# Performance work log

Hardware: AMD Instinct MI355X
Metric: run time of the kernel (lower is better)

The kernel has to match this reference:

```python
import jax, jax.numpy as jnp
import numpy as np

N_NODES = 10000
N_EDGES = 640000
IN_DIM = 128
HID = 128
N_GRAPHS = 64


def setup_inputs() -> dict:
    key = jax.random.key(0)
    ks = jax.random.split(key, 9)
    x = jax.random.normal(ks[0], (N_NODES, IN_DIM), dtype=jnp.float32)
    edge_index = jax.random.randint(ks[1], (2, N_EDGES), 0, N_NODES, dtype=jnp.int32)
    batch = jnp.sort(jax.random.randint(ks[2], (N_NODES,), 0, N_GRAPHS, dtype=jnp.int32))
    # GCNConv weights (glorot-ish init) and zero biases
    W0 = jax.random.normal(ks[3], (IN_DIM, HID), dtype=jnp.float32) / np.float32(np.sqrt(IN_DIM))
    b0 = jnp.zeros((HID,), dtype=jnp.float32)
    W1 = jax.random.normal(ks[4], (HID, HID), dtype=jnp.float32) / np.float32(np.sqrt(HID))
    b1 = jnp.zeros((HID,), dtype=jnp.float32)
    W2 = jax.random.normal(ks[5], (HID, HID), dtype=jnp.float32) / np.float32(np.sqrt(HID))
    b2 = jnp.zeros((HID,), dtype=jnp.float32)
    return {"x": x, "edge_index": edge_index, "batch": batch,
            "W0": W0, "b0": b0, "W1": W1, "b1": b1, "W2": W2, "b2": b2}


def _gcn_conv(x, src, dst, W, b, n_nodes):
    """PyG GCNConv: self-loops + symmetric normalization, then linear+bias."""
    h = x @ W  # [N, H]
    # degree of destination nodes, +1 for the added self-loop
    deg = jax.ops.segment_sum(jnp.ones((src.shape[0],), h.dtype), dst,
                              num_segments=n_nodes) + 1.0
    dis = jax.lax.rsqrt(deg)  # deg >= 1 so no inf guard needed
    # messages along real edges, normalized by dis[src]*dis[dst]
    msg = h[src] * (dis[src] * dis[dst])[:, None]  # [E, H]
    out = jax.ops.segment_sum(msg, dst, num_segments=n_nodes)
    # self-loop contribution: dis[i]^2 * h[i]
    out = out + h * (dis * dis)[:, None]
    return out + b


def reference(x, edge_index, batch, W0, b0, W1, b1, W2, b2):
    src, dst = edge_index[0], edge_index[1]
    n_nodes = x.shape[0]
    # layer 0 and 1 followed by ReLU (dropout: eval mode -> identity)
    h = _gcn_conv(x, src, dst, W0, b0, n_nodes)
    h = jax.nn.relu(h)
    h = _gcn_conv(h, src, dst, W1, b1, n_nodes)
    h = jax.nn.relu(h)
    h = _gcn_conv(h, src, dst, W2, b2, n_nodes)
    # global mean pool over batch indices
    sums = jax.ops.segment_sum(h, batch, num_segments=N_GRAPHS)  # [B, H]
    counts = jax.ops.segment_sum(jnp.ones((n_nodes,), h.dtype), batch,
                                 num_segments=N_GRAPHS)
    return sums / jnp.maximum(counts, 1.0)[:, None]
```

## Files before the change

kernel.cpp:

```cpp
#include <hip/hip_runtime.h>
#include <hip/hip_fp16.h>

#define NN 10000
#define NE 640000
#define NG 64
#define CAP 128
#define NB 625
#define BCAP 1280

typedef _Float16 f16x8 __attribute__((ext_vector_type(8)));
typedef float f32x4 __attribute__((ext_vector_type(4)));

__global__ __launch_bounds__(256) void k_init(const int* __restrict__ batch,
                                              int* __restrict__ gstart,
                                              int* __restrict__ bcur,
                                              const float* __restrict__ W0,
                                              const float* __restrict__ W1,
                                              const float* __restrict__ W2,
                                              __half* __restrict__ wh,
                                              __half* __restrict__ wl) {
    int bid = blockIdx.x, t = threadIdx.x;
    if (bid < 40) {
        int i = bid * 256 + t;
        if (i < NB) bcur[i] = 0;
        if (i >= NN) return;
        int b = batch[i];
        int prev = (i == 0) ? -1 : batch[i - 1];
        for (int g = prev + 1; g <= b; g++) gstart[g] = i;
        if (i == NN - 1)
            for (int g = b + 1; g <= NG; g++) gstart[g] = NN;
        return;
    }
    int wid = bid - 40;
    int z = wid >> 6;
    int q = (wid & 63) * 256 + t;
    int c = q >> 7, k = q & 127;
    const float* W = (z == 0) ? W0 : (z == 1) ? W1 : W2;
    float v = W[k * 128 + c];
    __half h = __float2half(v);
    __half lo = __float2half(v - __half2float(h));
    wh[z * 16384 + c * 128 + k] = h;
    wl[z * 16384 + c * 128 + k] = lo;
}

__global__ __launch_bounds__(256) void k_p1(const int* __restrict__ ei,
                                            int* __restrict__ bcur,
                                            int* __restrict__ pk) {
    __shared__ int hist[NB];
    int t = threadIdx.x;
    for (int q = t; q < NB; q += 256) hist[q] = 0;
    __syncthreads();

    int4 s4[4], d4[4];
    int ebase = blockIdx.x * 4096;
#pragma unroll
    for (int q = 0; q < 4; q++) {
        int e = ebase + q * 1024 + t * 4;
        if (e < NE) {
            s4[q] = *(const int4*)&ei[e];
            d4[q] = *(const int4*)&ei[NE + e];
            atomicAdd(&hist[d4[q].x >> 4], 1);
            atomicAdd(&hist[d4[q].y >> 4], 1);
            atomicAdd(&hist[d4[q].z >> 4], 1);
            atomicAdd(&hist[d4[q].w >> 4], 1);
        }
    }
    __syncthreads();

    for (int q = t; q < NB; q += 256) {
        int h = hist[q];
        hist[q] = (h > 0) ? atomicAdd(&bcur[q], h) : 0;
    }
    __syncthreads();

#pragma unroll
    for (int q = 0; q < 4; q++) {
        int e = ebase + q * 1024 + t * 4;
        if (e < NE) {
            int b0 = d4[q].x >> 4, b1 = d4[q].y >> 4, b2 = d4[q].z >> 4, b3 = d4[q].w >> 4;
            int r0 = atomicAdd(&hist[b0], 1);
            int r1 = atomicAdd(&hist[b1], 1);
            int r2 = atomicAdd(&hist[b2], 1);
            int r3 = atomicAdd(&hist[b3], 1);
            if (r0 < BCAP) pk[b0 * BCAP + r0] = s4[q].x | ((d4[q].x & 15) << 14);
            if (r1 < BCAP) pk[b1 * BCAP + r1] = s4[q].y | ((d4[q].y & 15) << 14);
            if (r2 < BCAP) pk[b2 * BCAP + r2] = s4[q].z | ((d4[q].z & 15) << 14);
            if (r3 < BCAP) pk[b3 * BCAP + r3] = s4[q].w | ((d4[q].w & 15) << 14);
        }
    }
}

__global__ __launch_bounds__(256) void k_p2(const int* __restrict__ bcur,
                                            const int* __restrict__ pk,
                                            int* __restrict__ deg,
                                            int* __restrict__ csrc) {
    __shared__ int buf[16 * CAP];
    __shared__ int cnt[16];
    int b = blockIdx.x, t = threadIdx.x;
    if (t < 16) cnt[t] = 0;
    __syncthreads();

    int n = bcur[b];
    if (n > BCAP) n = BCAP;
    const int* pb = &pk[b * BCAP];
    for (int i = t; i < n; i += 256) {
        int v = pb[i];
        int nd = v >> 14;
        int slot = atomicAdd(&cnt[nd], 1);
        if (slot < CAP) buf[(nd << 7) + slot] = v & 0x3FFF;
    }
    __syncthreads();

    int node0 = b << 4;
    if (t < 16) {
        int c = cnt[t];
        deg[node0 + t] = c;
        buf[(t << 7) + min(c, CAP - 1)] = NN;
    }
    __syncthreads();

    int4* d4 = (int4*)&csrc[node0 << 7];
    const int4* s4 = (const int4*)buf;
#pragma unroll
    for (int i = 0; i < 2; i++) d4[t + i * 256] = s4[t + i * 256];
}

__global__ __launch_bounds__(256) void k_gemm(const float* __restrict__ in,
                                              const __half* __restrict__ whT,
                                              const __half* __restrict__ wlT,
                                              const int* __restrict__ deg,
                                              __half* __restrict__ g16, int relu) {
    int t = threadIdx.x;
    int w = t >> 6, l = t & 63;
    int rw = blockIdx.x * 32 + (w & 1) * 16;
    int cw = blockIdx.y * 64 + (w >> 1) * 32;
    int lr = l & 15, lg = l >> 4;
    int row = rw + lr;
    int rclamp = min(row, NN - 1);
    const _Float16* wh = (const _Float16*)whT;
    const _Float16* wl = (const _Float16*)wlT;
    f32x4 acc0 = {0.f, 0.f, 0.f, 0.f}, acc1 = {0.f, 0.f, 0.f, 0.f};
#pragma unroll
    for (int ks = 0; ks < 4; ks++) {
        int kb = ks * 32 + lg * 8;
        float4 xa = *(const float4*)&in[rclamp * 128 + kb];
        float4 xb = *(const float4*)&in[rclamp * 128 + kb + 4];
        float x0 = xa.x, x1 = xa.y, x2 = xa.z, x3 = xa.w;
        float x4 = xb.x, x5 = xb.y, x6 = xb.z, x7 = xb.w;
        if (relu) {
            x0 = fmaxf(x0, 0.f); x1 = fmaxf(x1, 0.f); x2 = fmaxf(x2, 0.f); x3 = fmaxf(x3, 0.f);
            x4 = fmaxf(x4, 0.f); x5 = fmaxf(x5, 0.f); x6 = fmaxf(x6, 0.f); x7 = fmaxf(x7, 0.f);
        }
        f16x8 ah, al;
        ah[0] = (_Float16)x0; al[0] = (_Float16)(x0 - (float)ah[0]);
        ah[1] = (_Float16)x1; al[1] = (_Float16)(x1 - (float)ah[1]);
        ah[2] = (_Float16)x2; al[2] = (_Float16)(x2 - (float)ah[2]);
        ah[3] = (_Float16)x3; al[3] = (_Float16)(x3 - (float)ah[3]);
        ah[4] = (_Float16)x4; al[4] = (_Float16)(x4 - (float)ah[4]);
        ah[5] = (_Float16)x5; al[5] = (_Float16)(x5 - (float)ah[5]);
        ah[6] = (_Float16)x6; al[6] = (_Float16)(x6 - (float)ah[6]);
        ah[7] = (_Float16)x7; al[7] = (_Float16)(x7 - (float)ah[7]);
        int c0 = cw + lr;
        f16x8 bh0 = *(const f16x8*)&wh[c0 * 128 + kb];
        f16x8 bl0 = *(const f16x8*)&wl[c0 * 128 + kb];
        f16x8 bh1 = *(const f16x8*)&wh[(c0 + 16) * 128 + kb];
        f16x8 bl1 = *(const f16x8*)&wl[(c0 + 16) * 128 + kb];
        acc0 = __builtin_amdgcn_mfma_f32_16x16x32_f16(ah, bh0, acc0, 0, 0, 0);
        acc1 = __builtin_amdgcn_mfma_f32_16x16x32_f16(ah, bh1, acc1, 0, 0, 0);
        acc0 = __builtin_amdgcn_mfma_f32_16x16x32_f16(al, bh0, acc0, 0, 0, 0);
        acc1 = __builtin_amdgcn_mfma_f32_16x16x32_f16(al, bh1, acc1, 0, 0, 0);
        acc0 = __builtin_amdgcn_mfma_f32_16x16x32_f16(ah, bl0, acc0, 0, 0, 0);
        acc1 = __builtin_amdgcn_mfma_f32_16x16x32_f16(ah, bl1, acc1, 0, 0, 0);
    }
#pragma unroll
    for (int reg = 0; reg < 4; reg++) {
        int r = rw + lg * 4 + reg;
        int c = cw + lr;
        if (r < NN) {
            float d = rsqrtf((float)deg[r] + 1.0f);
            g16[r * 128 + c] = __float2half(acc0[reg] * d);
            g16[r * 128 + c + 16] = __float2half(acc1[reg] * d);
        } else {
            g16[r * 128 + c] = __float2half(0.f);
            g16[r * 128 + c + 16] = __float2half(0.f);
        }
    }
}

__device__ __forceinline__ void accp(uint2 v, float2& p, float2& q) {
    float2 f0 = __half22float2(*(__half2*)&v.x);
    float2 f1 = __half22float2(*(__half2*)&v.y);
    p.x += f0.x; p.y += f0.y; q.x += f1.x; q.y += f1.y;
}

__global__ __launch_bounds__(256) void k_agg(const __half* __restrict__ g16,
                                             const float* __restrict__ bias,
                                             const int* __restrict__ deg,
                                             const int* __restrict__ csrc,
                                             float* __restrict__ out) {
    int wid = blockIdx.x * 4 + (threadIdx.x >> 6);
    int l = threadIdx.x & 63;
    if (wid >= NN) return;
    int i = wid;
    int dgi = __builtin_amdgcn_readfirstlane(deg[i]);
    int n = min(dgi, CAP - 1);
    int np = (n + 1) & ~1;
    int half = l >> 5, li = l & 31;
    int co = li * 4;
    float2 A0 = {0.f, 0.f}, A1 = {0.f, 0.f};
    float2 B0 = {0.f, 0.f}, B1 = {0.f, 0.f};
    if (half == 0) {
        uint2 sv = *(const uint2*)&g16[i * 128 + co];
        float2 f0 = __half22float2(*(__half2*)&sv.x);
        float2 f1 = __half22float2(*(__half2*)&sv.y);
        A0 = f0; A1 = f1;
    }
    const int* cp = &csrc[i << 7];
    for (int base = 0; base < np; base += 64) {
        int m = np - base;
        if (m > 64) m = 64;
        int myedge = (l < m) ? cp[base + l] : NN;
        int pairs = m >> 1;
        int j = 0;
        for (; j + 8 <= pairs; j += 8) {
            int r0 = __shfl(myedge, 2 * j + half);
            int r1 = __shfl(myedge, 2 * j + 2 + half);
            int r2 = __shfl(myedge, 2 * j + 4 + half);
            int r3 = __shfl(myedge, 2 * j + 6 + half);
            int r4 = __shfl(myedge, 2 * j + 8 + half);
            int r5 = __shfl(myedge, 2 * j + 10 + half);
            int r6 = __shfl(myedge, 2 * j + 12 + half);
            int r7 = __shfl(myedge, 2 * j + 14 + half);
            uint2 v0 = *(const uint2*)&g16[r0 * 128 + co];
            uint2 v1 = *(const uint2*)&g16[r1 * 128 + co];
            uint2 v2 = *(const uint2*)&g16[r2 * 128 + co];
            uint2 v3 = *(const uint2*)&g16[r3 * 128 + co];
            uint2 v4 = *(const uint2*)&g16[r4 * 128 + co];
            uint2 v5 = *(const uint2*)&g16[r5 * 128 + co];
            uint2 v6 = *(const uint2*)&g16[r6 * 128 + co];
            uint2 v7 = *(const uint2*)&g16[r7 * 128 + co];
            accp(v0, A0, A1); accp(v1, B0, B1);
            accp(v2, A0, A1); accp(v3, B0, B1);
            accp(v4, A0, A1); accp(v5, B0, B1);
            accp(v6, A0, A1); accp(v7, B0, B1);
        }
        for (; j < pairs; j++) {
            int r = __shfl(myedge, 2 * j + half);
            uint2 v = *(const uint2*)&g16[r * 128 + co];
            accp(v, A0, A1);
        }
    }
    A0.x += B0.x; A0.y += B0.y; A1.x += B1.x; A1.y += B1.y;
    A0.x += __shfl_xor(A0.x, 32);
    A0.y += __shfl_xor(A0.y, 32);
    A1.x += __shfl_xor(A1.x, 32);
    A1.y += __shfl_xor(A1.y, 32);
    if (half == 0) {
        float di = rsqrtf((float)dgi + 1.0f);
        float4 bb = *(const float4*)&bias[co];
        float4 o;
        o.x = di * A0.x + bb.x;
        o.y = di * A0.y + bb.y;
        o.z = di * A1.x + bb.z;
        o.w = di * A1.y + bb.w;
        *(float4*)&out[i * 128 + co] = o;
    }
}

__global__ __launch_bounds__(256) void k_pool(const float* __restrict__ h,
                                              const int* __restrict__ gstart,
                                              float* __restrict__ out) {
    int g = blockIdx.x;
    int s = gstart[g], e = gstart[g + 1];
    int t = threadIdx.x;
    int c = t & 127, half = t >> 7;
    float acc = 0.f;
    for (int n = s + half; n < e; n += 2) acc += h[n * 128 + c];
    __shared__ float sm[256];
    sm[t] = acc;
    __syncthreads();
    if (half == 0) {
        float cnt = (float)max(e - s, 1);
        out[g * 128 + c] = (sm[c] + sm[128 + c]) / cnt;
    }
}

extern "C" void kernel_launch(void* const* d_in, const int* in_sizes, int n_in,
                              void* d_out, int out_size, void* d_ws, size_t ws_size,
                              hipStream_t stream) {
    const float* x     = (const float*)d_in[0];
    const int*   ei    = (const int*)d_in[1];
    const int*   batch = (const int*)d_in[2];
    const float* W0 = (const float*)d_in[3];
    const float* b0 = (const float*)d_in[4];
    const float* W1 = (const float*)d_in[5];
    const float* b1 = (const float*)d_in[6];
    const float* W2 = (const float*)d_in[7];
    const float* b2 = (const float*)d_in[8];
    float* out = (float*)d_out;

    float* ws    = (float*)d_ws;
    int*   deg   = (int*)ws;
    int*   gstart= (int*)(ws + 10240);
    int*   bcur  = (int*)(ws + 10320);
    int*   csrc  = (int*)(ws + 10960);
    __half* g16  = (__half*)(ws + 1290960);
    float* abuf  = ws + 1931984;
    int*   pk    = (int*)(ws + 1931984);
    __half* wh   = (__half*)(ws + 3211984);
    __half* wlo  = (__half*)(ws + 3236560);

    k_init<<<232, 256, 0, stream>>>(batch, gstart, bcur, W0, W1, W2, wh, wlo);
    k_p1<<<157, 256, 0, stream>>>(ei, bcur, pk);
    k_p2<<<NB, 256, 0, stream>>>(bcur, pk, deg, csrc);

    dim3 ggrid(313, 2);
    k_gemm<<<ggrid, 256, 0, stream>>>(x, wh, wlo, deg, g16, 0);
    k_agg<<<2500, 256, 0, stream>>>(g16, b0, deg, csrc, abuf);
    k_gemm<<<ggrid, 256, 0, stream>>>(abuf, wh + 16384, wlo + 16384, deg, g16, 1);
    k_agg<<<2500, 256, 0, stream>>>(g16, b1, deg, csrc, abuf);
    k_gemm<<<ggrid, 256, 0, stream>>>(abuf, wh + 32768, wlo + 32768, deg, g16, 1);
    k_agg<<<2500, 256, 0, stream>>>(g16, b2, deg, csrc, abuf);

    k_pool<<<NG, 256, 0, stream>>>(abuf, gstart, out);
}
```

Before: 197.4 us.

## Fuse edge bucketing with init, CSR build with first GEMM, aggregation with next GEMM

The setup kernel now also does the edge-bucketing pass, and the per-bucket CSR build also runs the first layer's split-fp16 MFMA GEMM. A new fused kernel aggregates 16 nodes into shared memory, applies bias and ReLU, then multiplies by the next layer's weights. This cuts the launch count and removes the fp32 activation round trip through global memory between aggregation and GEMM. The price is larger 512-thread blocks, per-block dependence on the slowest node's aggregation before the GEMM, and ping-pong fp16 buffers with explicitly zeroed sentinel rows.

```diff
diff --git a/kernel.cpp b/kernel.cpp
--- a/kernel.cpp
+++ b/kernel.cpp
@@ -11,89 +11,95 @@
 typedef _Float16 f16x8 __attribute__((ext_vector_type(8)));
 typedef float f32x4 __attribute__((ext_vector_type(4)));
 
-__global__ __launch_bounds__(256) void k_init(const int* __restrict__ batch,
-                                              int* __restrict__ gstart,
-                                              int* __restrict__ bcur,
-                                              const float* __restrict__ W0,
-                                              const float* __restrict__ W1,
-                                              const float* __restrict__ W2,
-                                              __half* __restrict__ wh,
-                                              __half* __restrict__ wl) {
+__device__ __forceinline__ void split8v(float4 xa, float4 xb, f16x8& ah, f16x8& al) {
+    float x[8] = {xa.x, xa.y, xa.z, xa.w, xb.x, xb.y, xb.z, xb.w};
+#pragma unroll
+    for (int j = 0; j < 8; j++) {
+        ah[j] = (_Float16)x[j];
+        al[j] = (_Float16)(x[j] - (float)ah[j]);
+    }
+}
+
+__global__ __launch_bounds__(256) void k_initp1(
+    const int* __restrict__ batch, int* __restrict__ gstart,
+    const float* __restrict__ W0, const float* __restrict__ W1, const float* __restrict__ W2,
+    __half* __restrict__ wh, __half* __restrict__ wl,
+    const int* __restrict__ ei, int* __restrict__ bcur, int* __restrict__ pk,
+    __half* __restrict__ g16a, __half* __restrict__ g16b)
+{
+    __shared__ int hist[NB];
     int bid = blockIdx.x, t = threadIdx.x;
     if (bid < 40) {
         int i = bid * 256 + t;
-        if (i < NB) bcur[i] = 0;
-        if (i >= NN) return;
-        int b = batch[i];
-        int prev = (i == 0) ? -1 : batch[i - 1];
-        for (int g = prev + 1; g <= b; g++) gstart[g] = i;
-        if (i == NN - 1)
-            for (int g = b + 1; g <= NG; g++) gstart[g] = NN;
-        return;
-    }
-    int wid = bid - 40;
-    int z = wid >> 6;
-    int q = (wid & 63) * 256 + t;
-    int c = q >> 7, k = q & 127;
-    const float* W = (z == 0) ? W0 : (z == 1) ? W1 : W2;
-    float v = W[k * 128 + c];
-    __half h = __float2half(v);
-    __half lo = __float2half(v - __half2float(h));
-    wh[z * 16384 + c * 128 + k] = h;
-    wl[z * 16384 + c * 128 + k] = lo;
-}
-
-__global__ __launch_bounds__(256) void k_p1(const int* __restrict__ ei,
-                                            int* __restrict__ bcur,
-                                            int* __restrict__ pk) {
-    __shared__ int hist[NB];
-    int t = threadIdx.x;
-    for (int q = t; q < NB; q += 256) hist[q] = 0;
-    __syncthreads();
-
-    int4 s4[4], d4[4];
-    int ebase = blockIdx.x * 4096;
-#pragma unroll
-    for (int q = 0; q < 4; q++) {
-        int e = ebase + q * 1024 + t * 4;
-        if (e < NE) {
-            s4[q] = *(const int4*)&ei[e];
-            d4[q] = *(const int4*)&ei[NE + e];
-            atomicAdd(&hist[d4[q].x >> 4], 1);
-            atomicAdd(&hist[d4[q].y >> 4], 1);
-            atomicAdd(&hist[d4[q].z >> 4], 1);
-            atomicAdd(&hist[d4[q].w >> 4], 1);
-        }
-    }
-    __syncthreads();
-
-    for (int q = t; q < NB; q += 256) {
-        int h = hist[q];
-        hist[q] = (h > 0) ? atomicAdd(&bcur[q], h) : 0;
-    }
-    __syncthreads();
-
-#pragma unroll
-    for (int q = 0; q < 4; q++) {
-        int e = ebase + q * 1024 + t * 4;
-        if (e < NE) {
-            int b0 = d4[q].x >> 4, b1 = d4[q].y >> 4, b2 = d4[q].z >> 4, b3 = d4[q].w >> 4;
-            int r0 = atomicAdd(&hist[b0], 1);
-            int r1 = atomicAdd(&hist[b1], 1);
-            int r2 = atomicAdd(&hist[b2], 1);
-            int r3 = atomicAdd(&hist[b3], 1);
-            if (r0 < BCAP) pk[b0 * BCAP + r0] = s4[q].x | ((d4[q].x & 15) << 14);
-            if (r1 < BCAP) pk[b1 * BCAP + r1] = s4[q].y | ((d4[q].y & 15) << 14);
-            if (r2 < BCAP) pk[b2 * BCAP + r2] = s4[q].z | ((d4[q].z & 15) << 14);
-            if (r3 < BCAP) pk[b3 * BCAP + r3] = s4[q].w | ((d4[q].w & 15) << 14);
-        }
-    }
-}
-
-__global__ __launch_bounds__(256) void k_p2(const int* __restrict__ bcur,
-                                            const int* __restrict__ pk,
-                                            int* __restrict__ deg,
-                                            int* __restrict__ csrc) {
+        if (i < NN) {
+            int b = batch[i];
+            int prev = (i == 0) ? -1 : batch[i - 1];
+            for (int g = prev + 1; g <= b; g++) gstart[g] = i;
+            if (i == NN - 1)
+                for (int g = b + 1; g <= NG; g++) gstart[g] = NN;
+        }
+    } else if (bid < 232) {
+        int wid = bid - 40;
+        int z = wid >> 6;
+        int q = (wid & 63) * 256 + t;
+        int c = q >> 7, k = q & 127;
+        const float* W = (z == 0) ? W0 : (z == 1) ? W1 : W2;
+        float v = W[k * 128 + c];
+        __half h = __float2half(v);
+        __half lo = __float2half(v - __half2float(h));
+        wh[z * 16384 + c * 128 + k] = h;
+        wl[z * 16384 + c * 128 + k] = lo;
+    } else if (bid < 389) {
+        for (int q = t; q < NB; q += 256) hist[q] = 0;
+        __syncthreads();
+        int4 s4[4], d4[4];
+        int ebase = (bid - 232) * 4096;
+#pragma unroll
+        for (int q = 0; q < 4; q++) {
+            int e = ebase + q * 1024 + t * 4;
+            if (e < NE) {
+                s4[q] = *(const int4*)&ei[e];
+                d4[q] = *(const int4*)&ei[NE + e];
+                atomicAdd(&hist[d4[q].x >> 4], 1);
+                atomicAdd(&hist[d4[q].y >> 4], 1);
+                atomicAdd(&hist[d4[q].z >> 4], 1);
+                atomicAdd(&hist[d4[q].w >> 4], 1);
+            }
+        }
+        __syncthreads();
+        for (int q = t; q < NB; q += 256) {
+            int h = hist[q];
+            hist[q] = (h > 0) ? atomicAdd(&bcur[q], h) : 0;
+        }
+        __syncthreads();
+#pragma unroll
+        for (int q = 0; q < 4; q++) {
+            int e = ebase + q * 1024 + t * 4;
+            if (e < NE) {
+                int b0i = d4[q].x >> 4, b1i = d4[q].y >> 4, b2i = d4[q].z >> 4, b3i = d4[q].w >> 4;
+                int r0 = atomicAdd(&hist[b0i], 1);
+                int r1 = atomicAdd(&hist[b1i], 1);
+                int r2 = atomicAdd(&hist[b2i], 1);
+                int r3 = atomicAdd(&hist[b3i], 1);
+                if (r0 < BCAP) pk[b0i * BCAP + r0] = s4[q].x | ((d4[q].x & 15) << 14);
+                if (r1 < BCAP) pk[b1i * BCAP + r1] = s4[q].y | ((d4[q].y & 15) << 14);
+                if (r2 < BCAP) pk[b2i * BCAP + r2] = s4[q].z | ((d4[q].z & 15) << 14);
+                if (r3 < BCAP) pk[b3i * BCAP + r3] = s4[q].w | ((d4[q].w & 15) << 14);
+            }
+        }
+    } else {
+        uint4 z = {0u, 0u, 0u, 0u};
+        ((uint4*)(g16a + NN * 128))[t] = z;
+        ((uint4*)(g16b + NN * 128))[t] = z;
+    }
+}
+
+__global__ __launch_bounds__(512) void k_p2g0(
+    const int* __restrict__ bcur, const int* __restrict__ pk,
+    const float* __restrict__ x,
+    const __half* __restrict__ whT, const __half* __restrict__ wlT,
+    int* __restrict__ deg, int* __restrict__ csrc, __half* __restrict__ g16a)
+{
     __shared__ int buf[16 * CAP];
     __shared__ int cnt[16];
     int b = blockIdx.x, t = threadIdx.x;
@@ -103,7 +109,7 @@
     int n = bcur[b];
     if (n > BCAP) n = BCAP;
     const int* pb = &pk[b * BCAP];
-    for (int i = t; i < n; i += 256) {
+    for (int i = t; i < n; i += 512) {
         int v = pb[i];
         int nd = v >> 14;
         int slot = atomicAdd(&cnt[nd], 1);
@@ -119,71 +125,31 @@
     }
     __syncthreads();
 
-    int4* d4 = (int4*)&csrc[node0 << 7];
-    const int4* s4 = (const int4*)buf;
-#pragma unroll
-    for (int i = 0; i < 2; i++) d4[t + i * 256] = s4[t + i * 256];
-}
-
-__global__ __launch_bounds__(256) void k_gemm(const float* __restrict__ in,
-                                              const __half* __restrict__ whT,
-                                              const __half* __restrict__ wlT,
-                                              const int* __restrict__ deg,
-                                              __half* __restrict__ g16, int relu) {
-    int t = threadIdx.x;
-    int w = t >> 6, l = t & 63;
-    int rw = blockIdx.x * 32 + (w & 1) * 16;
-    int cw = blockIdx.y * 64 + (w >> 1) * 32;
-    int lr = l & 15, lg = l >> 4;
-    int row = rw + lr;
-    int rclamp = min(row, NN - 1);
-    const _Float16* wh = (const _Float16*)whT;
-    const _Float16* wl = (const _Float16*)wlT;
-    f32x4 acc0 = {0.f, 0.f, 0.f, 0.f}, acc1 = {0.f, 0.f, 0.f, 0.f};
+    ((int4*)&csrc[node0 << 7])[t] = ((const int4*)buf)[t];
+
+    int w = t >> 6, l = t & 63, lr = l & 15, lg = l >> 4;
+    int cw = w * 16;
+    const _Float16* whp = (const _Float16*)whT;
+    const _Float16* wlp = (const _Float16*)wlT;
+    f32x4 acc = {0.f, 0.f, 0.f, 0.f};
 #pragma unroll
     for (int ks = 0; ks < 4; ks++) {
         int kb = ks * 32 + lg * 8;
-        float4 xa = *(const float4*)&in[rclamp * 128 + kb];
-        float4 xb = *(const float4*)&in[rclamp * 128 + kb + 4];
-        float x0 = xa.x, x1 = xa.y, x2 = xa.z, x3 = xa.w;
-        float x4 = xb.x, x5 = xb.y, x6 = xb.z, x7 = xb.w;
-        if (relu) {
-            x0 = fmaxf(x0, 0.f); x1 = fmaxf(x1, 0.f); x2 = fmaxf(x2, 0.f); x3 = fmaxf(x3, 0.f);
-            x4 = fmaxf(x4, 0.f); x5 = fmaxf(x5, 0.f); x6 = fmaxf(x6, 0.f); x7 = fmaxf(x7, 0.f);
-        }
         f16x8 ah, al;
-        ah[0] = (_Float16)x0; al[0] = (_Float16)(x0 - (float)ah[0]);
-        ah[1] = (_Float16)x1; al[1] = (_Float16)(x1 - (float)ah[1]);
-        ah[2] = (_Float16)x2; al[2] = (_Float16)(x2 - (float)ah[2]);
-        ah[3] = (_Float16)x3; al[3] = (_Float16)(x3 - (float)ah[3]);
-        ah[4] = (_Float16)x4; al[4] = (_Float16)(x4 - (float)ah[4]);
-        ah[5] = (_Float16)x5; al[5] = (_Float16)(x5 - (float)ah[5]);
-        ah[6] = (_Float16)x6; al[6] = (_Float16)(x6 - (float)ah[6]);
-        ah[7] = (_Float16)x7; al[7] = (_Float16)(x7 - (float)ah[7]);
+        split8v(*(const float4*)&x[(node0 + lr) * 128 + kb],
+                *(const float4*)&x[(node0 + lr) * 128 + kb + 4], ah, al);
         int c0 = cw + lr;
-        f16x8 bh0 = *(const f16x8*)&wh[c0 * 128 + kb];
-        f16x8 bl0 = *(const f16x8*)&wl[c0 * 128 + kb];
-        f16x8 bh1 = *(const f16x8*)&wh[(c0 + 16) * 128 + kb];
-        f16x8 bl1 = *(const f16x8*)&wl[(c0 + 16) * 128 + kb];
-        acc0 = __builtin_amdgcn_mfma_f32_16x16x32_f16(ah, bh0, acc0, 0, 0, 0);
-        acc1 = __builtin_amdgcn_mfma_f32_16x16x32_f16(ah, bh1, acc1, 0, 0, 0);
-        acc0 = __builtin_amdgcn_mfma_f32_16x16x32_f16(al, bh0, acc0, 0, 0, 0);
-        acc1 = __builtin_amdgcn_mfma_f32_16x16x32_f16(al, bh1, acc1, 0, 0, 0);
-        acc0 = __builtin_amdgcn_mfma_f32_16x16x32_f16(ah, bl0, acc0, 0, 0, 0);
-        acc1 = __builtin_amdgcn_mfma_f32_16x16x32_f16(ah, bl1, acc1, 0, 0, 0);
+        f16x8 bh = *(const f16x8*)&whp[c0 * 128 + kb];
+        f16x8 bl = *(const f16x8*)&wlp[c0 * 128 + kb];
+        acc = __builtin_amdgcn_mfma_f32_16x16x32_f16(ah, bh, acc, 0, 0, 0);
+        acc = __builtin_amdgcn_mfma_f32_16x16x32_f16(al, bh, acc, 0, 0, 0);
+        acc = __builtin_amdgcn_mfma_f32_16x16x32_f16(ah, bl, acc, 0, 0, 0);
     }
 #pragma unroll
     for (int reg = 0; reg < 4; reg++) {
-        int r = rw + lg * 4 + reg;
-        int c = cw + lr;
-        if (r < NN) {
-            float d = rsqrtf((float)deg[r] + 1.0f);
-            g16[r * 128 + c] = __float2half(acc0[reg] * d);
-            g16[r * 128 + c + 16] = __float2half(acc1[reg] * d);
-        } else {
-            g16[r * 128 + c] = __float2half(0.f);
-            g16[r * 128 + c + 16] = __float2half(0.f);
-        }
+        int row = lg * 4 + reg;
+        float d = rsqrtf((float)cnt[row] + 1.0f);
+        g16a[(node0 + row) * 128 + cw + lr] = __float2half(acc[reg] * d);
     }
 }
 
@@ -191,6 +157,110 @@
     float2 f0 = __half22float2(*(__half2*)&v.x);
     float2 f1 = __half22float2(*(__half2*)&v.y);
     p.x += f0.x; p.y += f0.y; q.x += f1.x; q.y += f1.y;
+}
+
+__global__ __launch_bounds__(512) void k_ag(
+    const __half* __restrict__ gin, const float* __restrict__ bias,
+    const int* __restrict__ deg, const int* __restrict__ csrc,
+    const __half* __restrict__ whT, const __half* __restrict__ wlT,
+    __half* __restrict__ gout)
+{
+    __shared__ float Xs[16][132];
+    int base = blockIdx.x << 4;
+    int t = threadIdx.x;
+    int w = t >> 6, l = t & 63;
+    int half = l >> 5, li = l & 31;
+    int co = li * 4;
+#pragma unroll
+    for (int k4 = 0; k4 < 2; k4++) {
+        int row = w * 2 + k4;
+        int i = base + row;
+        int dgi = __builtin_amdgcn_readfirstlane(deg[i]);
+        int nn_ = min(dgi, CAP - 1);
+        int np = (nn_ + 1) & ~1;
+        float2 A0 = {0.f, 0.f}, A1 = {0.f, 0.f};
+        float2 B0 = {0.f, 0.f}, B1 = {0.f, 0.f};
+        if (half == 0) {
+            uint2 sv = *(const uint2*)&gin[i * 128 + co];
+            A0 = __half22float2(*(__half2*)&sv.x);
+            A1 = __half22float2(*(__half2*)&sv.y);
+        }
+        const int* cp = &csrc[i << 7];
+        for (int bs = 0; bs < np; bs += 64) {
+            int m = np - bs;
+            if (m > 64) m = 64;
+            int myedge = (l < m) ? cp[bs + l] : NN;
+            int pairs = m >> 1;
+            int j = 0;
+            for (; j + 8 <= pairs; j += 8) {
+                int r0 = __shfl(myedge, 2 * j + half);
+                int r1 = __shfl(myedge, 2 * j + 2 + half);
+                int r2 = __shfl(myedge, 2 * j + 4 + half);
+                int r3 = __shfl(myedge, 2 * j + 6 + half);
+                int r4 = __shfl(myedge, 2 * j + 8 + half);
+                int r5 = __shfl(myedge, 2 * j + 10 + half);
+                int r6 = __shfl(myedge, 2 * j + 12 + half);
+                int r7 = __shfl(myedge, 2 * j + 14 + half);
+                uint2 v0 = *(const uint2*)&gin[r0 * 128 + co];
+                uint2 v1 = *(const uint2*)&gin[r1 * 128 + co];
+                uint2 v2 = *(const uint2*)&gin[r2 * 128 + co];
+                uint2 v3 = *(const uint2*)&gin[r3 * 128 + co];
+                uint2 v4 = *(const uint2*)&gin[r4 * 128 + co];
+                uint2 v5 = *(const uint2*)&gin[r5 * 128 + co];
+                uint2 v6 = *(const uint2*)&gin[r6 * 128 + co];
+                uint2 v7 = *(const uint2*)&gin[r7 * 128 + co];
+                accp(v0, A0, A1); accp(v1, B0, B1);
+                accp(v2, A0, A1); accp(v3, B0, B1);
+                accp(v4, A0, A1); accp(v5, B0, B1);
+                accp(v6, A0, A1); accp(v7, B0, B1);
+            }
+            for (; j < pairs; j++) {
+                int r = __shfl(myedge, 2 * j + half);
+                uint2 v = *(const uint2*)&gin[r * 128 + co];
+                accp(v, A0, A1);
+            }
+        }
+        A0.x += B0.x; A0.y += B0.y; A1.x += B1.x; A1.y += B1.y;
+        A0.x += __shfl_xor(A0.x, 32);
+        A0.y += __shfl_xor(A0.y, 32);
+        A1.x += __shfl_xor(A1.x, 32);
+        A1.y += __shfl_xor(A1.y, 32);
+        if (half == 0) {
+            float di = rsqrtf((float)dgi + 1.0f);
+            float4 bb = *(const float4*)&bias[co];
+            float4 o;
+            o.x = fmaxf(di * A0.x + bb.x, 0.f);
+            o.y = fmaxf(di * A0.y + bb.y, 0.f);
+            o.z = fmaxf(di * A1.x + bb.z, 0.f);
+            o.w = fmaxf(di * A1.y + bb.w, 0.f);
+            *(float4*)&Xs[row][co] = o;
+        }
+    }
+    __syncthreads();
+
+    int lr = l & 15, lg = l >> 4;
+    int cw = w * 16;
+    const _Float16* whp = (const _Float16*)whT;
+    const _Float16* wlp = (const _Float16*)wlT;
+    f32x4 acc = {0.f, 0.f, 0.f, 0.f};
+#pragma unroll
+    for (int ks = 0; ks < 4; ks++) {
+        int kb = ks * 32 + lg * 8;
+        f16x8 ah, al;
+        split8v(*(const float4*)&Xs[lr][kb], *(const float4*)&Xs[lr][kb + 4], ah, al);
+        int c0 = cw + lr;
+        f16x8 bh = *(const f16x8*)&whp[c0 * 128 + kb];
+        f16x8 bl = *(const f16x8*)&wlp[c0 * 128 + kb];
+        acc = __builtin_amdgcn_mfma_f32_16x16x32_f16(ah, bh, acc, 0, 0, 0);
+        acc = __builtin_amdgcn_mfma_f32_16x16x32_f16(al, bh, acc, 0, 0, 0);
+        acc = __builtin_amdgcn_mfma_f32_16x16x32_f16(ah, bl, acc, 0, 0, 0);
+    }
+#pragma unroll
+    for (int reg = 0; reg < 4; reg++) {
+        int row = lg * 4 + reg;
+        float d = rsqrtf((float)deg[base + row] + 1.0f);
+        gout[(base + row) * 128 + cw + lr] = __float2half(acc[reg] * d);
+    }
 }
 
 __global__ __launch_bounds__(256) void k_agg(const __half* __restrict__ g16,
@@ -211,9 +281,8 @@
     float2 B0 = {0.f, 0.f}, B1 = {0.f, 0.f};
     if (half == 0) {
         uint2 sv = *(const uint2*)&g16[i * 128 + co];
-        float2 f0 = __half22float2(*(__half2*)&sv.x);
-        float2 f1 = __half22float2(*(__half2*)&sv.y);
-        A0 = f0; A1 = f1;
+        A0 = __half22float2(*(__half2*)&sv.x);
+        A1 = __half22float2(*(__half2*)&sv.y);
     }
     const int* cp = &csrc[i << 7];
     for (int base = 0; base < np; base += 64) {
@@ -304,23 +373,19 @@
     int*   gstart= (int*)(ws + 10240);
     int*   bcur  = (int*)(ws + 10320);
     int*   csrc  = (int*)(ws + 10960);
-    __half* g16  = (__half*)(ws + 1290960);
-    float* abuf  = ws + 1931984;
-    int*   pk    = (int*)(ws + 1931984);
-    __half* wh   = (__half*)(ws + 3211984);
-    __half* wlo  = (__half*)(ws + 3236560);
-
-    k_init<<<232, 256, 0, stream>>>(batch, gstart, bcur, W0, W1, W2, wh, wlo);
-    k_p1<<<157, 256, 0, stream>>>(ei, bcur, pk);
-    k_p2<<<NB, 256, 0, stream>>>(bcur, pk, deg, csrc);
-
-    dim3 ggrid(313, 2);
-    k_gemm<<<ggrid, 256, 0, stream>>>(x, wh, wlo, deg, g16, 0);
-    k_agg<<<2500, 256, 0, stream>>>(g16, b0, deg, csrc, abuf);
-    k_gemm<<<ggrid, 256, 0, stream>>>(abuf, wh + 16384, wlo + 16384, deg, g16, 1);
-    k_agg<<<2500, 256, 0, stream>>>(g16, b1, deg, csrc, abuf);
-    k_gemm<<<ggrid, 256, 0, stream>>>(abuf, wh + 32768, wlo + 32768, deg, g16, 1);
-    k_agg<<<2500, 256, 0, stream>>>(g16, b2, deg, csrc, abuf);
-
+    __half* g16a = (__half*)(ws + 1290960);
+    __half* g16b = (__half*)(ws + 1931984);
+    float* abuf  = ws + 2573008;
+    int*   pk    = (int*)(ws + 2573008);
+    __half* wh   = (__half*)(ws + 3853008);
+    __half* wlo  = (__half*)(ws + 3877584);
+
+    hipMemsetAsync(bcur, 0, 640 * sizeof(int), stream);
+    k_initp1<<<390, 256, 0, stream>>>(batch, gstart, W0, W1, W2, wh, wlo, ei, bcur, pk,
+                                      g16a, g16b);
+    k_p2g0<<<NB, 512, 0, stream>>>(bcur, pk, x, wh, wlo, deg, csrc, g16a);
+    k_ag<<<NB, 512, 0, stream>>>(g16a, b0, deg, csrc, wh + 16384, wlo + 16384, g16b);
+    k_ag<<<NB, 512, 0, stream>>>(g16b, b1, deg, csrc, wh + 32768, wlo + 32768, g16a);
+    k_agg<<<2500, 256, 0, stream>>>(g16a, b2, deg, csrc, abuf);
     k_pool<<<NG, 256, 0, stream>>>(abuf, gstart, out);
 }
```

Measured after the change: 184.7 us. 1.07x faster.
